# Optimization experiments

Measured on AMD Instinct MI355X. Metric: run time of the kernel, lower is better.

The kernel has to match this reference:

```python
import jax, jax.numpy as jnp
import numpy as np

TAU = 0.02
B, C, H, W = 8, 64, 256, 256


def setup_inputs() -> dict:
    key = jax.random.key(0)
    k1, k2, k3, k4, k5 = jax.random.split(key, 5)
    x = jax.random.normal(k1, (B, C, H, W), dtype=jnp.float32)
    # learned per-channel parameters (theta_a initialized near -4.0 as in the module,
    # small noise added so gradients/behavior are non-degenerate)
    theta_a = -4.0 + 0.1 * jax.random.normal(k2, (1, C, 1, 1), dtype=jnp.float32)
    theta_bx = 0.1 * jax.random.normal(k3, (1, C, 1, 1), dtype=jnp.float32)
    theta_by = 0.1 * jax.random.normal(k4, (1, C, 1, 1), dtype=jnp.float32)
    theta_c = 0.1 * jax.random.normal(k5, (1, C, 1, 1), dtype=jnp.float32)
    # base grid in normalized [-1,1] coords (align_corners=True convention)
    gy, gx = jnp.meshgrid(jnp.linspace(-1.0, 1.0, H, dtype=jnp.float32),
                          jnp.linspace(-1.0, 1.0, W, dtype=jnp.float32), indexing='ij')
    return {"x": x, "theta_a": theta_a, "theta_bx": theta_bx, "theta_by": theta_by,
            "theta_c": theta_c, "base_gx": gx, "base_gy": gy}


def _bilinear_shift_sample(x, base_gx, base_gy, sx, sy):
    """Bilinear grid_sample with border padding, align_corners=True,
    where the grid is base_grid shifted by a per-channel constant (sx, sy).
    x: [B,C,H,W]; base_gx/base_gy: [H,W]; sx, sy: [C] normalized shifts.
    Returns [B,C,H,W]."""
    gx = base_gx[None, :, :] + sx[:, None, None]          # [C,H,W]
    gy = base_gy[None, :, :] + sy[:, None, None]          # [C,H,W]
    # normalized -> pixel coords (align_corners=True), border padding = clamp
    px = jnp.clip((gx + 1.0) * 0.5 * (W - 1), 0.0, float(W - 1))
    py = jnp.clip((gy + 1.0) * 0.5 * (H - 1), 0.0, float(H - 1))
    x0f = jnp.floor(px)
    y0f = jnp.floor(py)
    wx = px - x0f                                          # [C,H,W]
    wy = py - y0f
    x0 = x0f.astype(jnp.int32)
    y0 = y0f.astype(jnp.int32)
    x1 = jnp.minimum(x0 + 1, W - 1)
    y1 = jnp.minimum(y0 + 1, H - 1)
    cidx = jnp.arange(C)[:, None, None]                    # [C,1,1]
    v00 = x[:, cidx, y0, x0]                               # [B,C,H,W]
    v01 = x[:, cidx, y0, x1]
    v10 = x[:, cidx, y1, x0]
    v11 = x[:, cidx, y1, x1]
    return (1.0 - wy) * ((1.0 - wx) * v00 + wx * v01) + wy * ((1.0 - wx) * v10 + wx * v11)


def reference(x, theta_a, theta_bx, theta_by, theta_c, base_gx, base_gy):
    a = jax.nn.softplus(theta_a)                           # [1,C,1,1]
    s = jnp.sqrt(a * TAU + 1e-8).reshape(C)                # diffusion shift per channel
    dx = (theta_bx * TAU).reshape(C)                       # drift shift per channel
    dy = (theta_by * TAU).reshape(C)
    u_px = _bilinear_shift_sample(x, base_gx, base_gy, s + dx, dy)
    u_nx = _bilinear_shift_sample(x, base_gx, base_gy, -s + dx, dy)
    u_py = _bilinear_shift_sample(x, base_gx, base_gy, dx, s + dy)
    u_ny = _bilinear_shift_sample(x, base_gx, base_gy, dx, -s + dy)
    evolution = 0.25 * (u_px + u_nx + u_py + u_ny)
    return evolution + TAU * theta_c * x
```

## Files before the change

kernel.cpp:

```cpp
#include <hip/hip_runtime.h>

#define TAU 0.02f

constexpr int Bc = 8, Cc = 64, Hc = 256, Wc = 256;
constexpr int R  = 32;
constexpr int NR = 40;

__device__ __forceinline__ void coordf(float g, float shift, int n,
                                       int& i0, int& i1, float& w) {
    float p = (g + shift + 1.0f) * (0.5f * (float)(n - 1));
    p = fminf(fmaxf(p, 0.0f), (float)(n - 1));
    float f = floorf(p);
    w  = p - f;
    i0 = (int)f;
    i1 = min(i0 + 1, n - 1);
}

__device__ __forceinline__ void coord_adj(float g, float shift, int n,
                                          int& m, float& w) {
    int i0, i1; float ww;
    coordf(g, shift, n, i0, i1, ww);
    const bool top = (i0 == n - 1);
    m = top ? n - 2 : i0;
    w = top ? 1.0f  : ww;
}

__device__ __forceinline__ float gy_of(int i) {
    return fmaf((float)i, 2.0f / 255.0f, -1.0f);
}

__device__ __forceinline__ float rdlane_f(float v, int lane) {
    return __int_as_float(__builtin_amdgcn_readlane(__float_as_int(v), lane));
}

__global__ __launch_bounds__(256, 4) void remizov_rl(
    const float* __restrict__ x,
    const float* __restrict__ th_a,
    const float* __restrict__ th_bx,
    const float* __restrict__ th_by,
    const float* __restrict__ th_c,
    const float* __restrict__ base_gx,
    const float* __restrict__ base_gy,
    float* __restrict__ out)
{
    __shared__ float tile[NR * Wc];

    const int j  = threadIdx.x;
    const int i0 = blockIdx.x * R;
    const int c  = blockIdx.y;
    const int b  = blockIdx.z;

    const float a  = log1pf(expf(th_a[c]));
    const float s  = sqrtf(a * TAU + 1e-8f);
    const float dx = th_bx[c] * TAU;
    const float dy = th_by[c] * TAU;
    const float tc = th_c[c]  * TAU;

    int   m_yc, m_yp, m_yn;
    float m_wc, m_wp, m_wn;
    {
        const float gyr = gy_of(i0 + (j & 31));
        coord_adj(gyr,      dy, Hc, m_yc, m_wc);
        coord_adj(gyr,  s + dy, Hc, m_yp, m_wp);
        coord_adj(gyr, -s + dy, Hc, m_yn, m_wn);
    }

    int rlo = min(i0, min(min(__builtin_amdgcn_readlane(m_yc, 0),
                              __builtin_amdgcn_readlane(m_yp, 0)),
                              __builtin_amdgcn_readlane(m_yn, 0)));
    int rhi = max(i0 + R - 1, max(max(__builtin_amdgcn_readlane(m_yc, 31),
                                      __builtin_amdgcn_readlane(m_yp, 31)),
                                      __builtin_amdgcn_readlane(m_yn, 31)) + 1);
    const int nrows = rhi - rlo + 1;

    const float gxv = base_gx[j];
    int xp, xn, xc; float wxp, wxn, wxc;
    coord_adj(gxv,  s + dx, Wc, xp, wxp);
    coord_adj(gxv, -s + dx, Wc, xn, wxn);
    coord_adj(gxv,      dx, Wc, xc, wxc);

    const size_t plane = (size_t)(b * Cc + c) * (size_t)(Hc * Wc);
    float* __restrict__ dst = out + plane + (size_t)i0 * Wc + j;

    if (nrows > NR) {
        const float* __restrict__ P = x + plane;
        for (int r = 0; r < R; ++r) {
            const float gyr = gy_of(i0 + r);
            int yc, yp, yn; float wyc, wyp, wyn;
            coord_adj(gyr,      dy, Hc, yc, wyc);
            coord_adj(gyr,  s + dy, Hc, yp, wyp);
            coord_adj(gyr, -s + dy, Hc, yn, wyn);
            auto bilg = [&](int y0, float wy, int x0, float wx) -> float {
                const float* r0 = P + y0 * Wc;
                const float* r1 = r0 + Wc;
                float t0 = r0[x0] + wx * (r0[x0 + 1] - r0[x0]);
                float t1 = r1[x0] + wx * (r1[x0 + 1] - r1[x0]);
                return t0 + wy * (t1 - t0);
            };
            float v0 = bilg(yc, wyc, xp, wxp);
            float v1 = bilg(yc, wyc, xn, wxn);
            float v2 = bilg(yp, wyp, xc, wxc);
            float v3 = bilg(yn, wyn, xc, wxc);
            float xv = P[(i0 + r) * Wc + j];
            dst[r * Wc] = 0.25f * (v0 + v1 + v2 + v3) + tc * xv;
        }
        return;
    }

    {
        const float* __restrict__ src = x + plane + (size_t)rlo * Wc;
        const int total = nrows * Wc;
        for (int e = j * 4; e < total; e += 256 * 4) {
            *reinterpret_cast<float4*>(&tile[e]) =
                *reinterpret_cast<const float4*>(src + e);
        }
    }
    __syncthreads();

    auto Hl = [&](int rowf, int xm, float wx) -> float {
        float t0 = tile[rowf + xm];
        float t1 = tile[rowf + xm + 1];
        return t0 + wx * (t1 - t0);
    };

    const int xvbase = (i0 - rlo) * Wc + j;
    int pyc = -1000000, pyp = -1000000, pyn = -1000000;
    float A0 = 0, A1 = 0, B0 = 0, B1 = 0, C0 = 0, C1 = 0, D0 = 0, D1 = 0;

#pragma unroll
    for (int r = 0; r < R; ++r) {
        const int   yc  = __builtin_amdgcn_readlane(m_yc, r);
        const float wyc = rdlane_f(m_wc, r);
        const int   yp  = __builtin_amdgcn_readlane(m_yp, r);
        const float wyp = rdlane_f(m_wp, r);
        const int   yn  = __builtin_amdgcn_readlane(m_yn, r);
        const float wyn = rdlane_f(m_wn, r);

        const int bc = (yc - rlo) << 8;
        if (yc == pyc + 1) {
            A0 = A1; B0 = B1;
            A1 = Hl(bc + Wc, xp, wxp);
            B1 = Hl(bc + Wc, xn, wxn);
        } else if (yc != pyc) {
            A0 = Hl(bc,      xp, wxp); A1 = Hl(bc + Wc, xp, wxp);
            B0 = Hl(bc,      xn, wxn); B1 = Hl(bc + Wc, xn, wxn);
        }
        pyc = yc;

        const int bp = (yp - rlo) << 8;
        if (yp == pyp + 1) {
            C0 = C1; C1 = Hl(bp + Wc, xc, wxc);
        } else if (yp != pyp) {
            C0 = Hl(bp, xc, wxc); C1 = Hl(bp + Wc, xc, wxc);
        }
        pyp = yp;

        const int bn = (yn - rlo) << 8;
        if (yn == pyn + 1) {
            D0 = D1; D1 = Hl(bn + Wc, xc, wxc);
        } else if (yn != pyn) {
            D0 = Hl(bn, xc, wxc); D1 = Hl(bn + Wc, xc, wxc);
        }
        pyn = yn;

        const float v01 = (A0 + wyc * (A1 - A0)) + (B0 + wyc * (B1 - B0));
        const float v2  = C0 + wyp * (C1 - C0);
        const float v3  = D0 + wyn * (D1 - D0);
        const float xv  = tile[xvbase + (r << 8)];
        dst[(size_t)(r << 8)] = 0.25f * (v01 + v2 + v3) + tc * xv;
    }
}

extern "C" void kernel_launch(void* const* d_in, const int* in_sizes, int n_in,
                              void* d_out, int out_size, void* d_ws, size_t ws_size,
                              hipStream_t stream)
{
    const float* x       = (const float*)d_in[0];
    const float* th_a    = (const float*)d_in[1];
    const float* th_bx   = (const float*)d_in[2];
    const float* th_by   = (const float*)d_in[3];
    const float* th_c    = (const float*)d_in[4];
    const float* base_gx = (const float*)d_in[5];
    const float* base_gy = (const float*)d_in[6];
    float* out = (float*)d_out;

    dim3 grid(Hc / R, Cc, Bc);
    dim3 block(Wc);
    remizov_rl<<<grid, block, 0, stream>>>(x, th_a, th_bx, th_by, th_c,
                                           base_gx, base_gy, out);
}
```

Baseline: 274.8 us.

## Replace per-row branchy vertical interpolation with fixed-coefficient sliding stencil

Treats the vertical shift as a constant row offset per channel, so each output row becomes a fixed-coefficient stencil over a sliding window of horizontally interpolated rows (3 for the x-shifted pair, 9 for the y-shifted pair). This drops the per-row readlanes and data-dependent branches. Rows where the constant-offset assumption breaks, such as border clamping, are detected with a ballot mask and recomputed on a fallback path. The cost is extra FMAs on the mostly-zero coefficients and possible double writes for fallback rows.

```diff
diff --git a/kernel.cpp b/kernel.cpp
--- a/kernel.cpp
+++ b/kernel.cpp
@@ -33,7 +33,7 @@
     return __int_as_float(__builtin_amdgcn_readlane(__float_as_int(v), lane));
 }
 
-__global__ __launch_bounds__(256, 4) void remizov_rl(
+__global__ __launch_bounds__(256, 4) void remizov_sten(
     const float* __restrict__ x,
     const float* __restrict__ th_a,
     const float* __restrict__ th_bx,
@@ -117,57 +117,86 @@
     }
     __syncthreads();
 
-    auto Hl = [&](int rowf, int xm, float wx) -> float {
-        float t0 = tile[rowf + xm];
-        float t1 = tile[rowf + xm + 1];
+    const int acr = __builtin_amdgcn_readlane(m_yc, 16) - (i0 + 16);
+    const int apr = __builtin_amdgcn_readlane(m_yp, 16) - (i0 + 16);
+    const int anr = __builtin_amdgcn_readlane(m_yn, 16) - (i0 + 16);
+    const float wc = rdlane_f(m_wc, 16);
+    const float wp = rdlane_f(m_wp, 16);
+    const float wn = rdlane_f(m_wn, 16);
+
+    unsigned int mask;
+    {
+        const int lane = j & 31;
+        bool ok = (m_yc == i0 + lane + acr) &&
+                  (m_yp == i0 + lane + apr) &&
+                  (m_yn == i0 + lane + anr);
+        mask = (unsigned int)__ballot(ok);
+        if (acr < -1 || acr > 0 || apr > 3 || apr < -4 || anr < -4 || anr > 3)
+            mask = 0u;
+    }
+
+    float cA[3], cB[9];
+#pragma unroll
+    for (int k = 0; k < 3; ++k)
+        cA[k] = ((k == acr + 1) ? (1.0f - wc) : 0.0f) +
+                ((k == acr + 2) ? wc          : 0.0f);
+#pragma unroll
+    for (int k = 0; k < 9; ++k)
+        cB[k] = ((k == apr + 4) ? (1.0f - wp) : 0.0f) +
+                ((k == apr + 5) ? wp          : 0.0f) +
+                ((k == anr + 4) ? (1.0f - wn) : 0.0f) +
+                ((k == anr + 5) ? wn          : 0.0f);
+
+    auto ldH = [&](int row, int xm, float wx) -> float {
+        row = min(max(row, rlo), rhi);
+        const int base = (row - rlo) << 8;
+        float t0 = tile[base + xm], t1 = tile[base + xm + 1];
         return t0 + wx * (t1 - t0);
     };
+    auto ldS = [&](int row) -> float {
+        return ldH(row, xp, wxp) + ldH(row, xn, wxn);
+    };
+
+    float S0 = ldS(i0 - 1), S1 = ldS(i0), S2 = ldS(i0 + 1);
+    float W0 = ldH(i0 - 4, xc, wxc), W1 = ldH(i0 - 3, xc, wxc),
+          W2 = ldH(i0 - 2, xc, wxc), W3 = ldH(i0 - 1, xc, wxc),
+          W4 = ldH(i0,     xc, wxc), W5 = ldH(i0 + 1, xc, wxc),
+          W6 = ldH(i0 + 2, xc, wxc), W7 = ldH(i0 + 3, xc, wxc),
+          W8 = ldH(i0 + 4, xc, wxc);
 
     const int xvbase = (i0 - rlo) * Wc + j;
-    int pyc = -1000000, pyp = -1000000, pyn = -1000000;
-    float A0 = 0, A1 = 0, B0 = 0, B1 = 0, C0 = 0, C1 = 0, D0 = 0, D1 = 0;
 
 #pragma unroll
     for (int r = 0; r < R; ++r) {
-        const int   yc  = __builtin_amdgcn_readlane(m_yc, r);
-        const float wyc = rdlane_f(m_wc, r);
-        const int   yp  = __builtin_amdgcn_readlane(m_yp, r);
-        const float wyp = rdlane_f(m_wp, r);
-        const int   yn  = __builtin_amdgcn_readlane(m_yn, r);
-        const float wyn = rdlane_f(m_wn, r);
-
-        const int bc = (yc - rlo) << 8;
-        if (yc == pyc + 1) {
-            A0 = A1; B0 = B1;
-            A1 = Hl(bc + Wc, xp, wxp);
-            B1 = Hl(bc + Wc, xn, wxn);
-        } else if (yc != pyc) {
-            A0 = Hl(bc,      xp, wxp); A1 = Hl(bc + Wc, xp, wxp);
-            B0 = Hl(bc,      xn, wxn); B1 = Hl(bc + Wc, xn, wxn);
-        }
-        pyc = yc;
-
-        const int bp = (yp - rlo) << 8;
-        if (yp == pyp + 1) {
-            C0 = C1; C1 = Hl(bp + Wc, xc, wxc);
-        } else if (yp != pyp) {
-            C0 = Hl(bp, xc, wxc); C1 = Hl(bp + Wc, xc, wxc);
-        }
-        pyp = yp;
-
-        const int bn = (yn - rlo) << 8;
-        if (yn == pyn + 1) {
-            D0 = D1; D1 = Hl(bn + Wc, xc, wxc);
-        } else if (yn != pyn) {
-            D0 = Hl(bn, xc, wxc); D1 = Hl(bn + Wc, xc, wxc);
-        }
-        pyn = yn;
-
-        const float v01 = (A0 + wyc * (A1 - A0)) + (B0 + wyc * (B1 - B0));
-        const float v2  = C0 + wyp * (C1 - C0);
-        const float v3  = D0 + wyn * (D1 - D0);
-        const float xv  = tile[xvbase + (r << 8)];
-        dst[(size_t)(r << 8)] = 0.25f * (v01 + v2 + v3) + tc * xv;
+        float acc = cA[0] * S0 + cA[1] * S1 + cA[2] * S2
+                  + cB[0] * W0 + cB[1] * W1 + cB[2] * W2
+                  + cB[3] * W3 + cB[4] * W4 + cB[5] * W5
+                  + cB[6] * W6 + cB[7] * W7 + cB[8] * W8;
+        const float xv = tile[xvbase + (r << 8)];
+        dst[(size_t)(r << 8)] = 0.25f * acc + tc * xv;
+        if (r < R - 1) {
+            S0 = S1; S1 = S2; S2 = ldS(i0 + r + 2);
+            W0 = W1; W1 = W2; W2 = W3; W3 = W4; W4 = W5;
+            W5 = W6; W6 = W7; W7 = W8; W8 = ldH(i0 + r + 5, xc, wxc);
+        }
+    }
+
+    if (mask != 0xFFFFFFFFu) {
+        for (int r = 0; r < R; ++r) {
+            if ((mask >> r) & 1u) continue;
+            const float gyr = gy_of(i0 + r);
+            int yc, yp, yn; float wyc, wyp, wyn;
+            coord_adj(gyr,      dy, Hc, yc, wyc);
+            coord_adj(gyr,  s + dy, Hc, yp, wyp);
+            coord_adj(gyr, -s + dy, Hc, yn, wyn);
+            float v01 = (1.0f - wyc) * ldS(yc) + wyc * ldS(yc + 1);
+            float v2  = (1.0f - wyp) * ldH(yp,     xc, wxc)
+                      +         wyp  * ldH(yp + 1, xc, wxc);
+            float v3  = (1.0f - wyn) * ldH(yn,     xc, wxc)
+                      +         wyn  * ldH(yn + 1, xc, wxc);
+            const float xv = tile[xvbase + (r << 8)];
+            dst[(size_t)(r << 8)] = 0.25f * (v01 + v2 + v3) + tc * xv;
+        }
     }
 }
 
@@ -186,6 +215,6 @@
 
     dim3 grid(Hc / R, Cc, Bc);
     dim3 block(Wc);
-    remizov_rl<<<grid, block, 0, stream>>>(x, th_a, th_bx, th_by, th_c,
-                                           base_gx, base_gy, out);
-}
+    remizov_sten<<<grid, block, 0, stream>>>(x, th_a, th_bx, th_by, th_c,
+                                             base_gx, base_gy, out);
+}
```

New measurement: 255.4 us. 1.08x faster.
